# Kernel optimization log

Measured on AMD Instinct MI355X. Metric: run time of the kernel, lower is better.

Reference implementation:

```python
import jax, jax.numpy as jnp
import numpy as np

EPS = 1e-5

def _conv1d(x, w, b):
    # x: [B, T, Cin]; w: [Cout, Cin, K] (torch layout); padding=1, stride=1
    y = jax.lax.conv_general_dilated(
        x, jnp.transpose(w, (2, 1, 0)), window_strides=(1,), padding=[(1, 1)],
        dimension_numbers=('NWC', 'WIO', 'NWC'))
    return y + b

def _layernorm(x, g, b):
    mu = jnp.mean(x, axis=-1, keepdims=True)
    var = jnp.mean(jnp.square(x - mu), axis=-1, keepdims=True)
    return (x - mu) * jax.lax.rsqrt(var + EPS) * g + b

def _predictor(x, conv1_w, conv1_b, ln1_g, ln1_b, conv2_w, conv2_b, ln2_g, ln2_b, lin_w, lin_b):
    h = _layernorm(jax.nn.relu(_conv1d(x, conv1_w, conv1_b)), ln1_g, ln1_b)
    h = _layernorm(jax.nn.relu(_conv1d(h, conv2_w, conv2_b)), ln2_g, ln2_b)
    # linear to 1 channel, relu, squeeze -> [B, T]
    return jax.nn.relu(jnp.einsum('btf,f->bt', h, lin_w[:, 0]) + lin_b[0])

def _length_regulate(x, durations, mel_max_length):
    # Equivalent to the one-hot alignment matmul: output frame p of batch b
    # copies token k where cumsum(dur)[k-1] <= p < cumsum(dur)[k]; zeros beyond total.
    B, T, D = x.shape
    cum = jnp.cumsum(durations, axis=-1)                       # [B, T]
    frames = jnp.arange(mel_max_length, dtype=cum.dtype)       # [M]
    idx = jax.vmap(lambda c: jnp.searchsorted(c, frames, side='right'))(cum)  # [B, M]
    idx = jnp.clip(idx, 0, T - 1)
    out = jnp.take_along_axis(x, idx[..., None], axis=1)       # [B, M, D]
    mask = (frames[None, :] < cum[:, -1:])                     # [B, M]
    return out * mask[..., None].astype(x.dtype)

def setup_inputs() -> dict:
    key = jax.random.key(0)
    ks = jax.random.split(key, 8)
    B, T, D, F = 32, 512, 256, 256
    M = 3584  # mel_max_length >= max possible sum of durations (7 * 512)
    x = jax.random.normal(ks[0], (B, T, D), dtype=jnp.float32)
    target = jax.random.randint(ks[1], (B, T), 0, 8, dtype=jnp.int32)
    s = 0.02
    return {
        'x': x,
        'conv1_w': jax.random.normal(ks[2], (F, D, 3), jnp.float32) * s,
        'conv1_b': jnp.zeros((F,), jnp.float32),
        'ln1_g': jnp.ones((F,), jnp.float32),
        'ln1_b': jnp.zeros((F,), jnp.float32),
        'conv2_w': jax.random.normal(ks[3], (F, F, 3), jnp.float32) * s,
        'conv2_b': jnp.zeros((F,), jnp.float32),
        'ln2_g': jnp.ones((F,), jnp.float32),
        'ln2_b': jnp.zeros((F,), jnp.float32),
        'lin_w': jax.random.normal(ks[4], (F, 1), jnp.float32) * s,
        'lin_b': jnp.zeros((1,), jnp.float32),
        'target': target,
        'mel_max_length': M,
    }

def reference(x, conv1_w, conv1_b, ln1_g, ln1_b, conv2_w, conv2_b, ln2_g, ln2_b, lin_w, lin_b, target, mel_max_length):
    dur_pred = _predictor(x, conv1_w, conv1_b, ln1_g, ln1_b, conv2_w, conv2_b, ln2_g, ln2_b, lin_w, lin_b)
    output = _length_regulate(x, target, mel_max_length)
    return output, dur_pred
```

## Files before the change

kernel.cpp:

```cpp
#include <hip/hip_runtime.h>
#include <hip/hip_bf16.h>

typedef float f32x4 __attribute__((ext_vector_type(4)));
typedef __bf16 bf16x8 __attribute__((ext_vector_type(8)));

static __device__ __forceinline__ unsigned short f2bf(float f) {
    unsigned int u = __float_as_uint(f);
    unsigned int r = (u + 0x7fffu + ((u >> 16) & 1u)) >> 16;
    return (unsigned short)r;
}

static __device__ __forceinline__ void gll16(const void* g, void* l) {
    __builtin_amdgcn_global_load_lds(
        (const __attribute__((address_space(1))) unsigned int*)g,
        (__attribute__((address_space(3))) unsigned int*)l, 16, 0, 0);
}

__global__ __launch_bounds__(512) void prep(
    const float* __restrict__ w1, const float* __restrict__ w2,
    unsigned short* __restrict__ w1p, unsigned short* __restrict__ w2p,
    const int* __restrict__ tgt, short* __restrict__ idxT, int M)
{
    int blk = blockIdx.x;
    if (blk < 256) {
        int gi = blk * 512 + threadIdx.x;
        const float* w = (gi < 65536) ? w1 : w2;
        unsigned short* wp = (gi < 65536) ? w1p : w2p;
        int p = gi & 65535;
        int n = p >> 8, cin = p & 255;
        const float* src = w + (size_t)p * 3;
        float a[3] = {src[0], src[1], src[2]};
        int nb = n >> 4, nl = n & 15;
        int e = cin & 7, lhi = (cin >> 3) & 3, chi = cin >> 5;
        int base = nb * 512 + (lhi * 16 + nl) * 8 + e;
        #pragma unroll
        for (int kk = 0; kk < 3; ++kk)
            wp[(kk * 8 + chi) * 8192 + base] = f2bf(a[kk]);
    } else {
        __shared__ int s[512];
        int b = blk - 256, tid = threadIdx.x;
        int d = tgt[b * 512 + tid];
        s[tid] = d;
        __syncthreads();
        for (int off = 1; off < 512; off <<= 1) {
            int v = (tid >= off) ? s[tid - off] : 0;
            __syncthreads();
            s[tid] += v;
            __syncthreads();
        }
        int myend = s[tid];
        int mystart = myend - d;
        short* row = idxT + (size_t)b * M;
        for (int p = mystart; p < myend; ++p) row[p] = (short)tid;
        __syncthreads();
        int total = s[511];
        for (int p = total + tid; p < M; p += 512) row[p] = (short)-1;
    }
}

__global__ __launch_bounds__(512, 4) void fused(
    const float* __restrict__ x,
    const unsigned short* __restrict__ w1p, const float* __restrict__ b1,
    const float* __restrict__ g1, const float* __restrict__ be1,
    const unsigned short* __restrict__ w2p, const float* __restrict__ b2,
    const float* __restrict__ g2, const float* __restrict__ be2,
    const float* __restrict__ lw, const float* __restrict__ lb,
    float* __restrict__ dur, const short* __restrict__ idxT,
    float* __restrict__ out, int M)
{
    __shared__ __align__(16) unsigned short H[64 * 256];
    __shared__ __align__(16) unsigned short As[66 * 64];
    __shared__ __align__(16) unsigned short Bsm[2][8192];
    __shared__ float lnS[4][64], lnQ[4][64], lnD[4][64];

    const int tid = threadIdx.x;
    const int lane = tid & 63;
    const int wv = tid >> 6;

    if (blockIdx.x >= 288) {
        int gid = blockIdx.x - 288;
        int b = gid / 56;
        int r0 = (gid - b * 56) * 64;
        const short* row = idxT + (size_t)b * M;
        int id[8];
        #pragma unroll
        for (int i = 0; i < 8; ++i) id[i] = row[r0 + i * 8 + wv];
        #pragma unroll
        for (int i = 0; i < 8; ++i) {
            int m = r0 + i * 8 + wv;
            float4 v = make_float4(0.f, 0.f, 0.f, 0.f);
            if (id[i] >= 0)
                v = *reinterpret_cast<const float4*>(x + ((size_t)(b * 512 + id[i])) * 256 + lane * 4);
            *reinterpret_cast<float4*>(out + ((size_t)b * M + m) * 256 + lane * 4) = v;
        }
        return;
    }

    const int wmi = wv >> 2, wni = wv & 3;
    const int grp = lane >> 4, lr = lane & 15;
    const int b = blockIdx.x / 9;
    const int t0 = (blockIdx.x - b * 9) * 62;

    char* bs0 = (char*)&Bsm[0][0];
    #define STAGE_B(basep, ktg, buf) do {                                      \
        const char* _s = (const char*)(basep) + (ktg) * 16384 + wv * 2048 + lane * 16; \
        char* _d = bs0 + (buf) * 16384 + wv * 2048;                            \
        gll16(_s, _d); gll16(_s + 1024, _d + 1024);                            \
    } while (0)

    f32x4 acc[2][4] = {};
    int cur = 0;
    for (int h = 0; h < 4; ++h) {
        #pragma unroll
        for (int i = 0; i < 3; ++i) {
            int cc = i * 512 + tid;
            if (cc < 66 * 16) {
                int row = cc >> 4, ql = cc & 15;
                int tt = t0 - 2 + row;
                ushort4 o = make_ushort4(0, 0, 0, 0);
                if ((unsigned)tt < 512u) {
                    float4 v = *reinterpret_cast<const float4*>(
                        x + ((size_t)(b * 512 + tt)) * 256 + h * 64 + ql * 4);
                    o.x = f2bf(v.x); o.y = f2bf(v.y); o.z = f2bf(v.z); o.w = f2bf(v.w);
                }
                *reinterpret_cast<ushort4*>(&As[row * 64 + ((ql * 4) ^ ((row & 7) << 3))]) = o;
            }
        }
        if (h == 0) STAGE_B(w1p, 0, cur);
        __syncthreads();

        for (int j = 0; j < 6; ++j) {
            if (j < 5) {
                int jn = j + 1;
                STAGE_B(w1p, (jn >> 1) * 8 + h * 2 + (jn & 1), cur ^ 1);
            } else if (h < 3) {
                STAGE_B(w1p, (h + 1) * 2, cur ^ 1);
            } else {
                STAGE_B(w2p, 0, cur ^ 1);
            }
            const int kk = j >> 1, cbl = j & 1;
            bf16x8 af[2], bfr[4];
            #pragma unroll
            for (int mi = 0; mi < 2; ++mi) {
                int tr = wmi * 32 + mi * 16 + lr + kk;
                af[mi] = *reinterpret_cast<const bf16x8*>(
                    &As[tr * 64 + ((cbl * 32 + grp * 8) ^ ((tr & 7) << 3))]);
            }
            #pragma unroll
            for (int ni = 0; ni < 4; ++ni)
                bfr[ni] = *reinterpret_cast<const bf16x8*>(&Bsm[cur][(wni * 4 + ni) * 512 + lane * 8]);
            __builtin_amdgcn_s_setprio(1);
            #pragma unroll
            for (int mi = 0; mi < 2; ++mi)
                #pragma unroll
                for (int ni = 0; ni < 4; ++ni)
                    acc[mi][ni] = __builtin_amdgcn_mfma_f32_16x16x32_bf16(af[mi], bfr[ni], acc[mi][ni], 0, 0, 0);
            __builtin_amdgcn_s_setprio(0);
            __syncthreads();
            cur ^= 1;
        }
    }

    {
        float bcol[4], gcol[4], becol[4];
        #pragma unroll
        for (int ni = 0; ni < 4; ++ni) {
            int col = wni * 64 + ni * 16 + lr;
            bcol[ni] = b1[col]; gcol[ni] = g1[col]; becol[ni] = be1[col];
        }
        #pragma unroll
        for (int mi = 0; mi < 2; ++mi)
            #pragma unroll
            for (int ni = 0; ni < 4; ++ni)
                #pragma unroll
                for (int r = 0; r < 4; ++r)
                    acc[mi][ni][r] = fmaxf(acc[mi][ni][r] + bcol[ni], 0.f);

        #pragma unroll
        for (int mi = 0; mi < 2; ++mi)
            #pragma unroll
            for (int r = 0; r < 4; ++r) {
                float s = acc[mi][0][r] + acc[mi][1][r] + acc[mi][2][r] + acc[mi][3][r];
                float q = acc[mi][0][r] * acc[mi][0][r] + acc[mi][1][r] * acc[mi][1][r]
                        + acc[mi][2][r] * acc[mi][2][r] + acc[mi][3][r] * acc[mi][3][r];
                #pragma unroll
                for (int off = 1; off < 16; off <<= 1) {
                    s += __shfl_xor(s, off);
                    q += __shfl_xor(q, off);
                }
                if (lr == 0) {
                    int R = wmi * 32 + mi * 16 + grp * 4 + r;
                    lnS[wni][R] = s; lnQ[wni][R] = q;
                }
            }
        __syncthreads();
        #pragma unroll
        for (int mi = 0; mi < 2; ++mi)
            #pragma unroll
            for (int r = 0; r < 4; ++r) {
                int R = wmi * 32 + mi * 16 + grp * 4 + r;
                int t = t0 - 1 + R;
                float valid = ((unsigned)t < 512u) ? 1.f : 0.f;
                float mu = (lnS[0][R] + lnS[1][R] + lnS[2][R] + lnS[3][R]) * (1.f / 256.f);
                float var = (lnQ[0][R] + lnQ[1][R] + lnQ[2][R] + lnQ[3][R]) * (1.f / 256.f) - mu * mu;
                float rs = rsqrtf(var + 1e-5f);
                #pragma unroll
                for (int ni = 0; ni < 4; ++ni) {
                    int col = wni * 64 + ni * 16 + lr;
                    float hv = ((acc[mi][ni][r] - mu) * rs * gcol[ni] + becol[ni]) * valid;
                    H[R * 256 + (col ^ ((R & 7) << 3))] = f2bf(hv);
                }
            }
        __syncthreads();
    }

    f32x4 acc2[2][4] = {};
    for (int h = 0; h < 4; ++h) {
        for (int j = 0; j < 6; ++j) {
            if (j < 5) {
                int jn = j + 1;
                STAGE_B(w2p, (jn >> 1) * 8 + h * 2 + (jn & 1), cur ^ 1);
            } else if (h < 3) {
                STAGE_B(w2p, (h + 1) * 2, cur ^ 1);
            }
            const int kk = j >> 1, cbl = j & 1;
            bf16x8 af[2], bfr[4];
            #pragma unroll
            for (int mi = 0; mi < 2; ++mi) {
                int tr = wmi * 32 + mi * 16 + lr + kk - 1;
                int trc = tr < 0 ? 0 : (tr > 63 ? 63 : tr);
                af[mi] = *reinterpret_cast<const bf16x8*>(
                    &H[trc * 256 + ((h * 64 + cbl * 32 + grp * 8) ^ ((trc & 7) << 3))]);
            }
            #pragma unroll
            for (int ni = 0; ni < 4; ++ni)
                bfr[ni] = *reinterpret_cast<const bf16x8*>(&Bsm[cur][(wni * 4 + ni) * 512 + lane * 8]);
            __builtin_amdgcn_s_setprio(1);
            #pragma unroll
            for (int mi = 0; mi < 2; ++mi)
                #pragma unroll
                for (int ni = 0; ni < 4; ++ni)
                    acc2[mi][ni] = __builtin_amdgcn_mfma_f32_16x16x32_bf16(af[mi], bfr[ni], acc2[mi][ni], 0, 0, 0);
            __builtin_amdgcn_s_setprio(0);
            __syncthreads();
            cur ^= 1;
        }
    }

    {
        float bcol[4], gcol[4], becol[4], wcol[4];
        #pragma unroll
        for (int ni = 0; ni < 4; ++ni) {
            int col = wni * 64 + ni * 16 + lr;
            bcol[ni] = b2[col]; gcol[ni] = g2[col]; becol[ni] = be2[col]; wcol[ni] = lw[col];
        }
        #pragma unroll
        for (int mi = 0; mi < 2; ++mi)
            #pragma unroll
            for (int ni = 0; ni < 4; ++ni)
                #pragma unroll
                for (int r = 0; r < 4; ++r)
                    acc2[mi][ni][r] = fmaxf(acc2[mi][ni][r] + bcol[ni], 0.f);

        #pragma unroll
        for (int mi = 0; mi < 2; ++mi)
            #pragma unroll
            for (int r = 0; r < 4; ++r) {
                float s = acc2[mi][0][r] + acc2[mi][1][r] + acc2[mi][2][r] + acc2[mi][3][r];
                float q = acc2[mi][0][r] * acc2[mi][0][r] + acc2[mi][1][r] * acc2[mi][1][r]
                        + acc2[mi][2][r] * acc2[mi][2][r] + acc2[mi][3][r] * acc2[mi][3][r];
                #pragma unroll
                for (int off = 1; off < 16; off <<= 1) {
                    s += __shfl_xor(s, off);
                    q += __shfl_xor(q, off);
                }
                if (lr == 0) {
                    int R = wmi * 32 + mi * 16 + grp * 4 + r;
                    lnS[wni][R] = s; lnQ[wni][R] = q;
                }
            }
        __syncthreads();
        #pragma unroll
        for (int mi = 0; mi < 2; ++mi)
            #pragma unroll
            for (int r = 0; r < 4; ++r) {
                int R = wmi * 32 + mi * 16 + grp * 4 + r;
                float mu = (lnS[0][R] + lnS[1][R] + lnS[2][R] + lnS[3][R]) * (1.f / 256.f);
                float var = (lnQ[0][R] + lnQ[1][R] + lnQ[2][R] + lnQ[3][R]) * (1.f / 256.f) - mu * mu;
                float rs = rsqrtf(var + 1e-5f);
                float d = ((acc2[mi][0][r] - mu) * rs * gcol[0] + becol[0]) * wcol[0]
                        + ((acc2[mi][1][r] - mu) * rs * gcol[1] + becol[1]) * wcol[1]
                        + ((acc2[mi][2][r] - mu) * rs * gcol[2] + becol[2]) * wcol[2]
                        + ((acc2[mi][3][r] - mu) * rs * gcol[3] + becol[3]) * wcol[3];
                #pragma unroll
                for (int off = 1; off < 16; off <<= 1) d += __shfl_xor(d, off);
                if (lr == 0) lnD[wni][R] = d;
            }
        __syncthreads();
        if (tid < 64) {
            int R = tid;
            int t = t0 - 1 + R;
            if (R >= 1 && R <= 62 && t < 512) {
                float dd = lnD[0][R] + lnD[1][R] + lnD[2][R] + lnD[3][R] + lb[0];
                dur[(size_t)b * 512 + t] = fmaxf(dd, 0.f);
            }
        }
    }
    #undef STAGE_B
}

extern "C" void kernel_launch(void* const* d_in, const int* in_sizes, int n_in,
                              void* d_out, int out_size, void* d_ws, size_t ws_size,
                              hipStream_t stream) {
    const float* x   = (const float*)d_in[0];
    const float* w1  = (const float*)d_in[1];
    const float* b1  = (const float*)d_in[2];
    const float* g1  = (const float*)d_in[3];
    const float* be1 = (const float*)d_in[4];
    const float* w2  = (const float*)d_in[5];
    const float* b2  = (const float*)d_in[6];
    const float* g2  = (const float*)d_in[7];
    const float* be2 = (const float*)d_in[8];
    const float* lw  = (const float*)d_in[9];
    const float* lb  = (const float*)d_in[10];
    const int* tgt   = (const int*)d_in[11];
    float* out = (float*)d_out;

    const int B = 32, T = 512, C = 256;
    const int rows = B * T;
    const int M = (out_size - rows) / (B * C);

    char* ws = (char*)d_ws;
    unsigned short* w1p = (unsigned short*)(ws);
    unsigned short* w2p = (unsigned short*)(ws + 393216);
    short* idxT         = (short*)(ws + 786432);

    prep<<<288, 512, 0, stream>>>(w1, w2, w1p, w2p, tgt, idxT, M);
    fused<<<2080, 512, 0, stream>>>(x, w1p, b1, g1, be1, w2p, b2, g2, be2,
                                    lw, lb, out + (size_t)B * M * C, idxT, out, M);
}
```

Before: 53.55 us.

## Load packed weights directly from global into registers, dropping LDS double-buffer

Replaces the double-buffered LDS staging of packed conv weights (global_load_lds plus a barrier per k-step) with direct per-wave global loads of the pre-packed bf16 fragments into registers. This removes 32KB of shared memory and most __syncthreads in both GEMM phases, and fully unrolls the loops so the compiler can hoist loads. The trade-off is that each wave reads its weight fragments from L2/global with exposed latency and no explicit prefetch. The higher register pressure from unrolling may also hurt occupancy.

```diff
diff --git a/kernel.cpp b/kernel.cpp
--- a/kernel.cpp
+++ b/kernel.cpp
@@ -8,12 +8,6 @@
     unsigned int u = __float_as_uint(f);
     unsigned int r = (u + 0x7fffu + ((u >> 16) & 1u)) >> 16;
     return (unsigned short)r;
-}
-
-static __device__ __forceinline__ void gll16(const void* g, void* l) {
-    __builtin_amdgcn_global_load_lds(
-        (const __attribute__((address_space(1))) unsigned int*)g,
-        (__attribute__((address_space(3))) unsigned int*)l, 16, 0, 0);
 }
 
 __global__ __launch_bounds__(512) void prep(
@@ -70,7 +64,6 @@
 {
     __shared__ __align__(16) unsigned short H[64 * 256];
     __shared__ __align__(16) unsigned short As[66 * 64];
-    __shared__ __align__(16) unsigned short Bsm[2][8192];
     __shared__ float lnS[4][64], lnQ[4][64], lnD[4][64];
 
     const int tid = threadIdx.x;
@@ -101,15 +94,17 @@
     const int b = blockIdx.x / 9;
     const int t0 = (blockIdx.x - b * 9) * 62;
 
-    char* bs0 = (char*)&Bsm[0][0];
-    #define STAGE_B(basep, ktg, buf) do {                                      \
-        const char* _s = (const char*)(basep) + (ktg) * 16384 + wv * 2048 + lane * 16; \
-        char* _d = bs0 + (buf) * 16384 + wv * 2048;                            \
-        gll16(_s, _d); gll16(_s + 1024, _d + 1024);                            \
+    const int wfoff = (wni * 4) * 512 + lane * 8;
+
+    #define LOADW(dst, wp, ktg) do {                                           \
+        const unsigned short* _p = (wp) + (size_t)(ktg) * 8192 + wfoff;        \
+        dst[0] = *reinterpret_cast<const bf16x8*>(_p);                         \
+        dst[1] = *reinterpret_cast<const bf16x8*>(_p + 512);                   \
+        dst[2] = *reinterpret_cast<const bf16x8*>(_p + 1024);                  \
+        dst[3] = *reinterpret_cast<const bf16x8*>(_p + 1536);                  \
     } while (0)
 
     f32x4 acc[2][4] = {};
-    int cur = 0;
     for (int h = 0; h < 4; ++h) {
         #pragma unroll
         for (int i = 0; i < 3; ++i) {
@@ -126,39 +121,29 @@
                 *reinterpret_cast<ushort4*>(&As[row * 64 + ((ql * 4) ^ ((row & 7) << 3))]) = o;
             }
         }
-        if (h == 0) STAGE_B(w1p, 0, cur);
-        __syncthreads();
-
+        __syncthreads();
+
+        #pragma unroll
         for (int j = 0; j < 6; ++j) {
-            if (j < 5) {
-                int jn = j + 1;
-                STAGE_B(w1p, (jn >> 1) * 8 + h * 2 + (jn & 1), cur ^ 1);
-            } else if (h < 3) {
-                STAGE_B(w1p, (h + 1) * 2, cur ^ 1);
-            } else {
-                STAGE_B(w2p, 0, cur ^ 1);
-            }
             const int kk = j >> 1, cbl = j & 1;
-            bf16x8 af[2], bfr[4];
+            const int ktg = kk * 8 + h * 2 + cbl;
+            bf16x8 bw[4], af[2];
+            LOADW(bw, w1p, ktg);
             #pragma unroll
             for (int mi = 0; mi < 2; ++mi) {
                 int tr = wmi * 32 + mi * 16 + lr + kk;
                 af[mi] = *reinterpret_cast<const bf16x8*>(
                     &As[tr * 64 + ((cbl * 32 + grp * 8) ^ ((tr & 7) << 3))]);
             }
-            #pragma unroll
-            for (int ni = 0; ni < 4; ++ni)
-                bfr[ni] = *reinterpret_cast<const bf16x8*>(&Bsm[cur][(wni * 4 + ni) * 512 + lane * 8]);
             __builtin_amdgcn_s_setprio(1);
             #pragma unroll
             for (int mi = 0; mi < 2; ++mi)
                 #pragma unroll
                 for (int ni = 0; ni < 4; ++ni)
-                    acc[mi][ni] = __builtin_amdgcn_mfma_f32_16x16x32_bf16(af[mi], bfr[ni], acc[mi][ni], 0, 0, 0);
+                    acc[mi][ni] = __builtin_amdgcn_mfma_f32_16x16x32_bf16(af[mi], bw[ni], acc[mi][ni], 0, 0, 0);
             __builtin_amdgcn_s_setprio(0);
-            __syncthreads();
-            cur ^= 1;
-        }
+        }
+        __syncthreads();
     }
 
     {
@@ -215,16 +200,14 @@
     }
 
     f32x4 acc2[2][4] = {};
+    #pragma unroll
     for (int h = 0; h < 4; ++h) {
+        #pragma unroll
         for (int j = 0; j < 6; ++j) {
-            if (j < 5) {
-                int jn = j + 1;
-                STAGE_B(w2p, (jn >> 1) * 8 + h * 2 + (jn & 1), cur ^ 1);
-            } else if (h < 3) {
-                STAGE_B(w2p, (h + 1) * 2, cur ^ 1);
-            }
             const int kk = j >> 1, cbl = j & 1;
-            bf16x8 af[2], bfr[4];
+            const int ktg = kk * 8 + h * 2 + cbl;
+            bf16x8 bw[4], af[2];
+            LOADW(bw, w2p, ktg);
             #pragma unroll
             for (int mi = 0; mi < 2; ++mi) {
                 int tr = wmi * 32 + mi * 16 + lr + kk - 1;
@@ -232,18 +215,13 @@
                 af[mi] = *reinterpret_cast<const bf16x8*>(
                     &H[trc * 256 + ((h * 64 + cbl * 32 + grp * 8) ^ ((trc & 7) << 3))]);
             }
-            #pragma unroll
-            for (int ni = 0; ni < 4; ++ni)
-                bfr[ni] = *reinterpret_cast<const bf16x8*>(&Bsm[cur][(wni * 4 + ni) * 512 + lane * 8]);
             __builtin_amdgcn_s_setprio(1);
             #pragma unroll
             for (int mi = 0; mi < 2; ++mi)
                 #pragma unroll
                 for (int ni = 0; ni < 4; ++ni)
-                    acc2[mi][ni] = __builtin_amdgcn_mfma_f32_16x16x32_bf16(af[mi], bfr[ni], acc2[mi][ni], 0, 0, 0);
+                    acc2[mi][ni] = __builtin_amdgcn_mfma_f32_16x16x32_bf16(af[mi], bw[ni], acc2[mi][ni], 0, 0, 0);
             __builtin_amdgcn_s_setprio(0);
-            __syncthreads();
-            cur ^= 1;
         }
     }
 
@@ -306,7 +284,7 @@
             }
         }
     }
-    #undef STAGE_B
+    #undef LOADW
 }
 
 extern "C" void kernel_launch(void* const* d_in, const int* in_sizes, int n_in,
```

Measured after the change: 50.14 us. -6.4%, faster.
